# Optimization experiments

Hardware: AMD Instinct MI355X
Metric: run time of the kernel (lower is better)

## Reference

```python
import jax, jax.numpy as jnp
import numpy as np


def setup_inputs() -> dict:
    key = jax.random.key(0)
    B, C, H, W = 8, 64, 64, 64
    x = jax.random.normal(key, (B, C, H, W), dtype=jnp.float32)
    return {"x": x}


def reference(x) -> jnp.ndarray:
    # x: (B, C, H, W). Spatial self-attention over N = H*W positions with
    # Q = K = V = flattened x, no scaling, no projections (the Conv2d in the
    # original __init__ is never used in forward).
    B, C, H, W = x.shape
    N = H * W
    f = x.reshape(B, C, N)  # (B, C, N)
    # att[b, n, m] = sum_c f[b, c, n] * f[b, c, m]  -> (B, N, N)
    att = jnp.einsum('bcn,bcm->bnm', f, f)
    att = jax.nn.softmax(att, axis=-1)
    # outp[b, c, n] = sum_m f[b, c, m] * att[b, n, m]^T  (f_x @ att)
    outp = jnp.einsum('bcm,bmn->bcn', f, att).reshape(B, C, H, W)
    return x + outp
```

## Files before the change

### kernel.cpp

```cpp
#include <hip/hip_runtime.h>

typedef short v8s __attribute__((ext_vector_type(8)));
typedef short v4s __attribute__((ext_vector_type(4)));
typedef float v4f __attribute__((ext_vector_type(4)));

#define LOG2E 1.44269504088896340736f

#define WS_FBF_T 0u
#define WS_FBF   4194304u
#define WS_G     8388608u
#define WS_MAXN  8519680u
#define WS_NEED  8519712u

__device__ __forceinline__ unsigned short f2bf_rne(float f) {
  unsigned int u = __builtin_bit_cast(unsigned int, f);
  u += 0x7FFFu + ((u >> 16) & 1u);
  return (unsigned short)(u >> 16);
}

__global__ __launch_bounds__(256) void prep_kernel(
    const float* __restrict__ x, unsigned short* __restrict__ fbf_t,
    unsigned short* __restrict__ fbf, float* __restrict__ g, int* __restrict__ maxn) {
  __shared__ unsigned short T[64 * 72];
  __shared__ float red[16][64];
  const int t = threadIdx.x;
  const int b = blockIdx.x & 7;
  const int n0 = (blockIdx.x >> 3) << 6;
  const int nn = (t & 15) << 2;
  float ps0 = 0.f, ps1 = 0.f, ps2 = 0.f, ps3 = 0.f;
#pragma unroll
  for (int j = 0; j < 4; ++j) {
    int c = (t >> 4) + j * 16;
    size_t gidx = ((size_t)(b * 64 + c) << 12) + (unsigned)(n0 + nn);
    float4 v = *(const float4*)(x + gidx);
    ushort4 w;
    w.x = f2bf_rne(v.x); w.y = f2bf_rne(v.y); w.z = f2bf_rne(v.z); w.w = f2bf_rne(v.w);
    *(ushort4*)(fbf + gidx) = w;
    T[(nn + 0) * 72 + c] = w.x;
    T[(nn + 1) * 72 + c] = w.y;
    T[(nn + 2) * 72 + c] = w.z;
    T[(nn + 3) * 72 + c] = w.w;
    ps0 += v.x * v.x; ps1 += v.y * v.y; ps2 += v.z * v.z; ps3 += v.w * v.w;
  }
  red[t >> 4][nn + 0] = ps0; red[t >> 4][nn + 1] = ps1;
  red[t >> 4][nn + 2] = ps2; red[t >> 4][nn + 3] = ps3;
  __syncthreads();
  if (t < 64) {
    float gs = 0.f;
#pragma unroll
    for (int i = 0; i < 16; ++i) gs += red[i][t];
    g[b * 4096 + n0 + t] = gs;
    float m = gs;
    m = fmaxf(m, __shfl_xor(m, 1, 64));
    m = fmaxf(m, __shfl_xor(m, 2, 64));
    m = fmaxf(m, __shfl_xor(m, 4, 64));
    m = fmaxf(m, __shfl_xor(m, 8, 64));
    m = fmaxf(m, __shfl_xor(m, 16, 64));
    m = fmaxf(m, __shfl_xor(m, 32, 64));
    if (t == 0) atomicMax(maxn + b, __float_as_int(m));
  }
#pragma unroll
  for (int i = 0; i < 2; ++i) {
    int idx = t + i * 256;
    int n = idx >> 3, cs = (idx & 7) << 3;
    *(v8s*)(fbf_t + (((size_t)b << 12) + (unsigned)(n0 + n)) * 64 + cs) =
        *(const v8s*)&T[n * 72 + cs];
  }
}

__global__ __launch_bounds__(512, 2) void chanattn_main(
    const float* __restrict__ x, const unsigned short* __restrict__ fbf_t,
    const unsigned short* __restrict__ fbf, const float* __restrict__ g,
    const int* __restrict__ maxn, float* __restrict__ out) {
  __shared__ __align__(16) unsigned char smem[37888];
  unsigned short* sKt = (unsigned short*)smem;
  unsigned short* sVc = (unsigned short*)(smem + 18432);
  float* lred = (float*)(smem + 35840);

  const int tid = threadIdx.x;
  const int wave = tid >> 6, lane = tid & 63, quad = lane >> 4, l15 = lane & 15;
  const int qg = wave >> 2, kg = wave & 3;
  const int b = blockIdx.x & 7, qt = blockIdx.x >> 3;

  const unsigned short* fT = fbf_t + ((size_t)b << 18);
  const unsigned short* fV = fbf + ((size_t)b << 18);

  const int sKey = tid >> 3, sC = (tid & 7) << 3;
  const int vC = tid >> 4, vK = (tid & 15) << 3;
  const int vSlot = (vK & ~31) + ((vK & 8) ? 16 : 0) + ((vK & 16) ? 4 : 0);

#pragma unroll
  for (int i = 0; i < 2; ++i)
    *(v8s*)&sKt[(sKey + i * 64) * 72 + sC] =
        *(const v8s*)&fT[(size_t)(qt * 128 + sKey + i * 64) * 64 + sC];

  v8s pfk[2], pfv[2];
#pragma unroll
  for (int i = 0; i < 2; ++i)
    pfk[i] = *(const v8s*)&fT[(size_t)(sKey + i * 64) * 64 + sC];
#pragma unroll
  for (int i = 0; i < 2; ++i)
    pfv[i] = *(const v8s*)&fV[(size_t)(vC + i * 32) * 4096 + vK];

  __syncthreads();
  v8s bQ[4][2];
#pragma unroll
  for (int jq = 0; jq < 4; ++jq)
#pragma unroll
    for (int cs = 0; cs < 2; ++cs)
      bQ[jq][cs] = *(const v8s*)&sKt[(qg * 64 + jq * 16 + l15) * 72 + cs * 32 + quad * 8];

  float msc[4];
  {
    const float gmax = __int_as_float(maxn[b]);
#pragma unroll
    for (int jq = 0; jq < 4; ++jq) {
      int row = qt * 128 + qg * 64 + jq * 16 + l15;
      msc[jq] = __builtin_sqrtf(g[b * 4096 + row] * gmax) * LOG2E;
    }
  }
  __syncthreads();

#pragma unroll
  for (int i = 0; i < 2; ++i)
    *(v8s*)&sKt[(sKey + i * 64) * 72 + sC] = pfk[i];
#pragma unroll
  for (int i = 0; i < 2; ++i) {
    v4s lo, hi;
#pragma unroll
    for (int j = 0; j < 4; ++j) { lo[j] = pfv[i][j]; hi[j] = pfv[i][j + 4]; }
    *(v4s*)&sVc[(vC + i * 32) * 136 + vSlot] = lo;
    *(v4s*)&sVc[(vC + i * 32) * 136 + vSlot + 8] = hi;
  }

  v4f oacc[4][4];
  float rsum[4];
#pragma unroll
  for (int ct = 0; ct < 4; ++ct)
#pragma unroll
    for (int jq = 0; jq < 4; ++jq) oacc[ct][jq] = (v4f){0.f, 0.f, 0.f, 0.f};
#pragma unroll
  for (int jq = 0; jq < 4; ++jq) rsum[jq] = 0.f;

  for (int kt = 0; kt < 32; ++kt) {
    __syncthreads();

    if (kt + 1 < 32) {
      const int k0 = (kt + 1) * 128;
#pragma unroll
      for (int i = 0; i < 2; ++i)
        pfk[i] = *(const v8s*)&fT[(size_t)(k0 + sKey + i * 64) * 64 + sC];
#pragma unroll
      for (int i = 0; i < 2; ++i)
        pfv[i] = *(const v8s*)&fV[(size_t)(vC + i * 32) * 4096 + k0 + vK];
    }

    v8s aK[2][2];
#pragma unroll
    for (int t = 0; t < 2; ++t)
#pragma unroll
      for (int cs = 0; cs < 2; ++cs)
        aK[t][cs] =
            *(const v8s*)&sKt[(kg * 32 + t * 16 + l15) * 72 + cs * 32 + quad * 8];
    v8s aV[4];
#pragma unroll
    for (int ct = 0; ct < 4; ++ct)
      aV[ct] = *(const v8s*)&sVc[(ct * 16 + l15) * 136 + kg * 32 + quad * 8];

    __syncthreads();

    if (kt + 1 < 32) {
#pragma unroll
      for (int i = 0; i < 2; ++i)
        *(v8s*)&sKt[(sKey + i * 64) * 72 + sC] = pfk[i];
#pragma unroll
      for (int i = 0; i < 2; ++i) {
        v4s lo, hi;
#pragma unroll
        for (int j = 0; j < 4; ++j) { lo[j] = pfv[i][j]; hi[j] = pfv[i][j + 4]; }
        *(v4s*)&sVc[(vC + i * 32) * 136 + vSlot] = lo;
        *(v4s*)&sVc[(vC + i * 32) * 136 + vSlot + 8] = hi;
      }
    }

#pragma unroll
    for (int jq = 0; jq < 4; ++jq) {
      v4f s0 = (v4f){0.f, 0.f, 0.f, 0.f};
      v4f s1 = (v4f){0.f, 0.f, 0.f, 0.f};
#pragma unroll
      for (int cs = 0; cs < 2; ++cs) {
        s0 = __builtin_amdgcn_mfma_f32_16x16x32_bf16(aK[0][cs], bQ[jq][cs], s0, 0, 0, 0);
        s1 = __builtin_amdgcn_mfma_f32_16x16x32_bf16(aK[1][cs], bQ[jq][cs], s1, 0, 0, 0);
      }
      float p0[4], p1[4];
#pragma unroll
      for (int r = 0; r < 4; ++r) {
        p0[r] = __builtin_amdgcn_exp2f(__builtin_fmaf(s0[r], LOG2E, -msc[jq]));
        p1[r] = __builtin_amdgcn_exp2f(__builtin_fmaf(s1[r], LOG2E, -msc[jq]));
      }
      rsum[jq] += ((p0[0] + p0[1]) + (p0[2] + p0[3])) +
                  ((p1[0] + p1[1]) + (p1[2] + p1[3]));
      uint4 up;
      up.x = (__builtin_bit_cast(unsigned int, p0[1]) & 0xFFFF0000u) |
             (__builtin_bit_cast(unsigned int, p0[0]) >> 16);
      up.y = (__builtin_bit_cast(unsigned int, p0[3]) & 0xFFFF0000u) |
             (__builtin_bit_cast(unsigned int, p0[2]) >> 16);
      up.z = (__builtin_bit_cast(unsigned int, p1[1]) & 0xFFFF0000u) |
             (__builtin_bit_cast(unsigned int, p1[0]) >> 16);
      up.w = (__builtin_bit_cast(unsigned int, p1[3]) & 0xFFFF0000u) |
             (__builtin_bit_cast(unsigned int, p1[2]) >> 16);
      v8s bp = __builtin_bit_cast(v8s, up);
#pragma unroll
      for (int ct = 0; ct < 4; ++ct)
        oacc[ct][jq] =
            __builtin_amdgcn_mfma_f32_16x16x32_bf16(aV[ct], bp, oacc[ct][jq], 0, 0, 0);
    }
  }

#pragma unroll
  for (int jq = 0; jq < 4; ++jq) {
    float s = rsum[jq];
    s += __shfl_xor(s, 16, 64);
    s += __shfl_xor(s, 32, 64);
    rsum[jq] = s;
  }
  if (quad == 0) {
#pragma unroll
    for (int jq = 0; jq < 4; ++jq)
      lred[(qg * 64 + jq * 16 + l15) * 4 + kg] = rsum[jq];
  }
  __syncthreads();
  float inv[4];
#pragma unroll
  for (int jq = 0; jq < 4; ++jq) {
    const float4 lv = *(const float4*)&lred[(qg * 64 + jq * 16 + l15) * 4];
    inv[jq] = __builtin_amdgcn_rcpf((lv.x + lv.y) + (lv.z + lv.w));
  }

  float* Obuf = (float*)smem;
#pragma unroll
  for (int round = 0; round < 4; ++round) {
    if (kg == round) {
#pragma unroll
      for (int ct = 0; ct < 4; ++ct)
#pragma unroll
        for (int jq = 0; jq < 4; ++jq)
#pragma unroll
          for (int r = 0; r < 4; ++r) {
            float val = oacc[ct][jq][r] * inv[jq];
            float* p = &Obuf[(qg * 64 + ct * 16 + quad * 4 + r) * 68 + jq * 16 + l15];
            if (round == 0) *p = val; else *p += val;
          }
    }
    __syncthreads();
  }
#pragma unroll
  for (int j = 0; j < 4; ++j) {
    int idx = tid + j * 512;
    int qg2 = idx >> 10, c = (idx >> 4) & 63, q4 = idx & 15;
    const float4 o = *(const float4*)&Obuf[(qg2 * 64 + c) * 68 + q4 * 4];
    size_t gidx = ((size_t)(b * 64 + c) << 12) + (unsigned)(qt * 128 + qg2 * 64 + q4 * 4);
    const float4 xv = *(const float4*)(x + gidx);
    float4 rv;
    rv.x = xv.x + o.x; rv.y = xv.y + o.y; rv.z = xv.z + o.z; rv.w = xv.w + o.w;
    *(float4*)(out + gidx) = rv;
  }
}

__global__ __launch_bounds__(512) void
chanattn_fallback(const float* __restrict__ x, float* __restrict__ out) {
  __shared__ __align__(16) unsigned char smem[54272];
  unsigned short* sKt = (unsigned short*)smem;
  unsigned short* sVc = (unsigned short*)(smem + 18432);
  unsigned short* sP  = (unsigned short*)(smem + 35840);
  const int tid = threadIdx.x;
  const int wave = tid >> 6, lane = tid & 63, quad = lane >> 4, l15 = lane & 15;
  const int b = blockIdx.x & 7, qt = blockIdx.x >> 3;
  const float* fb = x + (size_t)b * (64 * 4096);
  const int skey = tid & 127, sc0 = (tid >> 7) << 4;
  {
    float vq[16];
#pragma unroll
    for (int j = 0; j < 16; ++j) vq[j] = fb[(sc0 + j) * 4096 + qt * 128 + skey];
    unsigned short us[16];
#pragma unroll
    for (int j = 0; j < 16; ++j) us[j] = f2bf_rne(vq[j]);
#pragma unroll
    for (int h = 0; h < 2; ++h) {
      v8s t;
#pragma unroll
      for (int j = 0; j < 8; ++j) t[j] = (short)us[h * 8 + j];
      *(v8s*)&sKt[skey * 72 + sc0 + h * 8] = t;
    }
  }
  float vk[16];
#pragma unroll
  for (int j = 0; j < 16; ++j) vk[j] = fb[(sc0 + j) * 4096 + skey];
  __syncthreads();
  v8s aq[2];
#pragma unroll
  for (int cs = 0; cs < 2; ++cs)
    aq[cs] = *(const v8s*)&sKt[(wave * 16 + l15) * 72 + cs * 32 + quad * 8];
  __syncthreads();
  v4f oacc[4];
#pragma unroll
  for (int ct = 0; ct < 4; ++ct) oacc[ct] = (v4f){0.f, 0.f, 0.f, 0.f};
  float m_run[4], l_run[4];
#pragma unroll
  for (int r = 0; r < 4; ++r) { m_run[r] = -3.0e38f; l_run[r] = 0.f; }
  unsigned short* sPw = sP + wave * (16 * 72);
  for (int kt = 0; kt < 32; ++kt) {
    {
      unsigned short us[16];
#pragma unroll
      for (int j = 0; j < 16; ++j) us[j] = f2bf_rne(vk[j]);
#pragma unroll
      for (int h = 0; h < 2; ++h) {
        v8s t;
#pragma unroll
        for (int j = 0; j < 8; ++j) t[j] = (short)us[h * 8 + j];
        *(v8s*)&sKt[skey * 72 + sc0 + h * 8] = t;
      }
#pragma unroll
      for (int j = 0; j < 16; ++j) sVc[(sc0 + j) * 136 + skey] = us[j];
    }
    __syncthreads();
    if (kt + 1 < 32) {
      const int m0 = (kt + 1) * 128;
#pragma unroll
      for (int j = 0; j < 16; ++j) vk[j] = fb[(sc0 + j) * 4096 + m0 + skey];
    }
    v4f sacc[8];
#pragma unroll
    for (int t = 0; t < 8; ++t) {
      v4f acc = (v4f){0.f, 0.f, 0.f, 0.f};
#pragma unroll
      for (int cs = 0; cs < 2; ++cs) {
        v8s bf = *(const v8s*)&sKt[(t * 16 + l15) * 72 + cs * 32 + quad * 8];
        acc = __builtin_amdgcn_mfma_f32_16x16x32_bf16(aq[cs], bf, acc, 0, 0, 0);
      }
      sacc[t] = acc;
    }
    float alpha[4], msc[4], rsum[4];
#pragma unroll
    for (int r = 0; r < 4; ++r) {
      float mv = sacc[0][r];
#pragma unroll
      for (int t = 1; t < 8; ++t) mv = fmaxf(mv, sacc[t][r]);
      mv = fmaxf(mv, __shfl_xor(mv, 8, 64));
      mv = fmaxf(mv, __shfl_xor(mv, 4, 64));
      mv = fmaxf(mv, __shfl_xor(mv, 2, 64));
      mv = fmaxf(mv, __shfl_xor(mv, 1, 64));
      float mnew = fmaxf(m_run[r], mv);
      alpha[r] = __builtin_amdgcn_exp2f((m_run[r] - mnew) * LOG2E);
      m_run[r] = mnew;
      msc[r] = mnew * LOG2E;
      l_run[r] *= alpha[r];
      rsum[r] = 0.f;
    }
#pragma unroll
    for (int ct = 0; ct < 4; ++ct)
#pragma unroll
      for (int r = 0; r < 4; ++r) oacc[ct][r] *= alpha[r];
#pragma unroll
    for (int half = 0; half < 2; ++half) {
#pragma unroll
      for (int t = half * 4; t < half * 4 + 4; ++t)
#pragma unroll
        for (int r = 0; r < 4; ++r) {
          float p = __builtin_amdgcn_exp2f(__builtin_fmaf(sacc[t][r], LOG2E, -msc[r]));
          rsum[r] += p;
          sPw[(quad * 4 + r) * 72 + (t - half * 4) * 16 + l15] = f2bf_rne(p);
        }
      asm volatile("s_waitcnt lgkmcnt(0)" ::: "memory");
#pragma unroll
      for (int ms = 0; ms < 2; ++ms) {
        v8s af = *(const v8s*)&sPw[l15 * 72 + ms * 32 + quad * 8];
#pragma unroll
        for (int ct = 0; ct < 4; ++ct) {
          v8s bf = *(const v8s*)&sVc[(ct * 16 + l15) * 136 + (half * 2 + ms) * 32 + quad * 8];
          oacc[ct] = __builtin_amdgcn_mfma_f32_16x16x32_bf16(af, bf, oacc[ct], 0, 0, 0);
        }
      }
      asm volatile("s_waitcnt lgkmcnt(0)" ::: "memory");
    }
#pragma unroll
    for (int r = 0; r < 4; ++r) {
      float s = rsum[r];
      s += __shfl_xor(s, 8, 64);
      s += __shfl_xor(s, 4, 64);
      s += __shfl_xor(s, 2, 64);
      s += __shfl_xor(s, 1, 64);
      l_run[r] += s;
    }
    __syncthreads();
  }
  float inv[4];
#pragma unroll
  for (int r = 0; r < 4; ++r) inv[r] = __builtin_amdgcn_rcpf(l_run[r]);
  float* sOt = (float*)smem;
#pragma unroll
  for (int ct = 0; ct < 4; ++ct)
#pragma unroll
    for (int r = 0; r < 4; ++r)
      sOt[(ct * 16 + l15) * 132 + wave * 16 + quad * 4 + r] = oacc[ct][r] * inv[r];
  __syncthreads();
#pragma unroll
  for (int j = 0; j < 4; ++j) {
    int idx = tid + j * 512;
    int nv = idx & 31, c = idx >> 5;
    float4 o = *(const float4*)&sOt[c * 132 + nv * 4];
    size_t gaddr = (size_t)b * (64 * 4096) + (size_t)c * 4096 + (size_t)(qt * 128 + nv * 4);
    float4 xv = *(const float4*)(x + gaddr);
    float4 res = make_float4(xv.x + o.x, xv.y + o.y, xv.z + o.z, xv.w + o.w);
    *(float4*)(out + gaddr) = res;
  }
}

extern "C" void kernel_launch(void* const* d_in, const int* in_sizes, int n_in,
                              void* d_out, int out_size, void* d_ws, size_t ws_size,
                              hipStream_t stream) {
  const float* xin = (const float*)d_in[0];
  float* out = (float*)d_out;
  if (ws_size >= (size_t)WS_NEED) {
    unsigned short* fbf_t = (unsigned short*)((char*)d_ws + WS_FBF_T);
    unsigned short* fbf = (unsigned short*)((char*)d_ws + WS_FBF);
    float* g = (float*)((char*)d_ws + WS_G);
    int* maxn = (int*)((char*)d_ws + WS_MAXN);
    hipMemsetAsync(maxn, 0, 8 * sizeof(int), stream);
    prep_kernel<<<dim3(512), dim3(256), 0, stream>>>(xin, fbf_t, fbf, g, maxn);
    chanattn_main<<<dim3(256), dim3(512), 0, stream>>>(xin, fbf_t, fbf, g, maxn, out);
  } else {
    chanattn_fallback<<<dim3(256), dim3(512), 0, stream>>>(xin, out);
  }
}
```

Before: 118.2 us.

## Double-buffer K/V tiles in LDS and replace atomic max with per-block partials

The main loop now keeps two LDS buffers for the key and value tiles. Each iteration runs one barrier instead of two, and global prefetch runs two tiles ahead, with the store for the next tile placed after the first query sub-tile's MFMAs. The per-batch max norm is no longer built with a memset plus atomicMax. Prep blocks write partial maxima that the main kernel reduces with wave shuffles. This removes a memset launch and the atomics, but nearly doubles LDS use per block (to 72KB), which may limit occupancy at two 512-thread blocks per CU.

```diff
diff --git a/kernel.cpp b/kernel.cpp
--- a/kernel.cpp
+++ b/kernel.cpp
@@ -9,8 +9,8 @@
 #define WS_FBF_T 0u
 #define WS_FBF   4194304u
 #define WS_G     8388608u
-#define WS_MAXN  8519680u
-#define WS_NEED  8519712u
+#define WS_BMAX  8519680u
+#define WS_NEED  8521728u
 
 __device__ __forceinline__ unsigned short f2bf_rne(float f) {
   unsigned int u = __builtin_bit_cast(unsigned int, f);
@@ -20,7 +20,7 @@
 
 __global__ __launch_bounds__(256) void prep_kernel(
     const float* __restrict__ x, unsigned short* __restrict__ fbf_t,
-    unsigned short* __restrict__ fbf, float* __restrict__ g, int* __restrict__ maxn) {
+    unsigned short* __restrict__ fbf, float* __restrict__ g, float* __restrict__ bmax) {
   __shared__ unsigned short T[64 * 72];
   __shared__ float red[16][64];
   const int t = threadIdx.x;
@@ -57,7 +57,7 @@
     m = fmaxf(m, __shfl_xor(m, 8, 64));
     m = fmaxf(m, __shfl_xor(m, 16, 64));
     m = fmaxf(m, __shfl_xor(m, 32, 64));
-    if (t == 0) atomicMax(maxn + b, __float_as_int(m));
+    if (t == 0) bmax[b * 64 + (blockIdx.x >> 3)] = m;
   }
 #pragma unroll
   for (int i = 0; i < 2; ++i) {
@@ -71,11 +71,12 @@
 __global__ __launch_bounds__(512, 2) void chanattn_main(
     const float* __restrict__ x, const unsigned short* __restrict__ fbf_t,
     const unsigned short* __restrict__ fbf, const float* __restrict__ g,
-    const int* __restrict__ maxn, float* __restrict__ out) {
-  __shared__ __align__(16) unsigned char smem[37888];
-  unsigned short* sKt = (unsigned short*)smem;
-  unsigned short* sVc = (unsigned short*)(smem + 18432);
-  float* lred = (float*)(smem + 35840);
+    const float* __restrict__ bmax, float* __restrict__ out) {
+  __shared__ __align__(16) unsigned char smem[73728];
+  unsigned short* sKtB = (unsigned short*)smem;
+  unsigned short* sVcB = (unsigned short*)(smem + 18432);
+  float* lred = (float*)(smem + 71680);
+  const int BUF = 17920;
 
   const int tid = threadIdx.x;
   const int wave = tid >> 6, lane = tid & 63, quad = lane >> 4, l15 = lane & 15;
@@ -89,11 +90,22 @@
   const int vC = tid >> 4, vK = (tid & 15) << 3;
   const int vSlot = (vK & ~31) + ((vK & 8) ? 16 : 0) + ((vK & 16) ? 4 : 0);
 
-#pragma unroll
-  for (int i = 0; i < 2; ++i)
-    *(v8s*)&sKt[(sKey + i * 64) * 72 + sC] =
+  float gm = bmax[b * 64 + lane];
+  gm = fmaxf(gm, __shfl_xor(gm, 1, 64));
+  gm = fmaxf(gm, __shfl_xor(gm, 2, 64));
+  gm = fmaxf(gm, __shfl_xor(gm, 4, 64));
+  gm = fmaxf(gm, __shfl_xor(gm, 8, 64));
+  gm = fmaxf(gm, __shfl_xor(gm, 16, 64));
+  gm = fmaxf(gm, __shfl_xor(gm, 32, 64));
+  float gq[4];
+#pragma unroll
+  for (int jq = 0; jq < 4; ++jq)
+    gq[jq] = g[b * 4096 + qt * 128 + qg * 64 + jq * 16 + l15];
+
+#pragma unroll
+  for (int i = 0; i < 2; ++i)
+    *(v8s*)&sKtB[(sKey + i * 64) * 72 + sC] =
         *(const v8s*)&fT[(size_t)(qt * 128 + sKey + i * 64) * 64 + sC];
-
   v8s pfk[2], pfv[2];
 #pragma unroll
   for (int i = 0; i < 2; ++i)
@@ -108,30 +120,29 @@
   for (int jq = 0; jq < 4; ++jq)
 #pragma unroll
     for (int cs = 0; cs < 2; ++cs)
-      bQ[jq][cs] = *(const v8s*)&sKt[(qg * 64 + jq * 16 + l15) * 72 + cs * 32 + quad * 8];
-
+      bQ[jq][cs] = *(const v8s*)&sKtB[(qg * 64 + jq * 16 + l15) * 72 + cs * 32 + quad * 8];
   float msc[4];
-  {
-    const float gmax = __int_as_float(maxn[b]);
-#pragma unroll
-    for (int jq = 0; jq < 4; ++jq) {
-      int row = qt * 128 + qg * 64 + jq * 16 + l15;
-      msc[jq] = __builtin_sqrtf(g[b * 4096 + row] * gmax) * LOG2E;
-    }
-  }
-  __syncthreads();
-
-#pragma unroll
-  for (int i = 0; i < 2; ++i)
-    *(v8s*)&sKt[(sKey + i * 64) * 72 + sC] = pfk[i];
+#pragma unroll
+  for (int jq = 0; jq < 4; ++jq) msc[jq] = __builtin_sqrtf(gq[jq] * gm) * LOG2E;
+  __syncthreads();
+
+#pragma unroll
+  for (int i = 0; i < 2; ++i)
+    *(v8s*)&sKtB[(sKey + i * 64) * 72 + sC] = pfk[i];
 #pragma unroll
   for (int i = 0; i < 2; ++i) {
     v4s lo, hi;
 #pragma unroll
     for (int j = 0; j < 4; ++j) { lo[j] = pfv[i][j]; hi[j] = pfv[i][j + 4]; }
-    *(v4s*)&sVc[(vC + i * 32) * 136 + vSlot] = lo;
-    *(v4s*)&sVc[(vC + i * 32) * 136 + vSlot + 8] = hi;
-  }
+    *(v4s*)&sVcB[(vC + i * 32) * 136 + vSlot] = lo;
+    *(v4s*)&sVcB[(vC + i * 32) * 136 + vSlot + 8] = hi;
+  }
+#pragma unroll
+  for (int i = 0; i < 2; ++i)
+    pfk[i] = *(const v8s*)&fT[(size_t)(128 + sKey + i * 64) * 64 + sC];
+#pragma unroll
+  for (int i = 0; i < 2; ++i)
+    pfv[i] = *(const v8s*)&fV[(size_t)(vC + i * 32) * 4096 + 128 + vK];
 
   v4f oacc[4][4];
   float rsum[4];
@@ -144,9 +155,68 @@
 
   for (int kt = 0; kt < 32; ++kt) {
     __syncthreads();
-
-    if (kt + 1 < 32) {
-      const int k0 = (kt + 1) * 128;
+    const int po = (kt & 1) * BUF;
+    const int pn = ((kt & 1) ^ 1) * BUF;
+
+    v8s aK[2][2];
+#pragma unroll
+    for (int t = 0; t < 2; ++t)
+#pragma unroll
+      for (int cs = 0; cs < 2; ++cs)
+        aK[t][cs] =
+            *(const v8s*)&sKtB[po + (kg * 32 + t * 16 + l15) * 72 + cs * 32 + quad * 8];
+    v8s aV[4];
+#pragma unroll
+    for (int ct = 0; ct < 4; ++ct)
+      aV[ct] = *(const v8s*)&sVcB[po + (ct * 16 + l15) * 136 + kg * 32 + quad * 8];
+
+    {
+      const int jq = 0;
+      v4f s0 = (v4f){0.f, 0.f, 0.f, 0.f}, s1 = (v4f){0.f, 0.f, 0.f, 0.f};
+#pragma unroll
+      for (int cs = 0; cs < 2; ++cs) {
+        s0 = __builtin_amdgcn_mfma_f32_16x16x32_bf16(aK[0][cs], bQ[jq][cs], s0, 0, 0, 0);
+        s1 = __builtin_amdgcn_mfma_f32_16x16x32_bf16(aK[1][cs], bQ[jq][cs], s1, 0, 0, 0);
+      }
+      float p0[4], p1[4];
+#pragma unroll
+      for (int r = 0; r < 4; ++r) {
+        p0[r] = __builtin_amdgcn_exp2f(__builtin_fmaf(s0[r], LOG2E, -msc[jq]));
+        p1[r] = __builtin_amdgcn_exp2f(__builtin_fmaf(s1[r], LOG2E, -msc[jq]));
+      }
+      rsum[jq] += ((p0[0] + p0[1]) + (p0[2] + p0[3])) +
+                  ((p1[0] + p1[1]) + (p1[2] + p1[3]));
+      uint4 up;
+      up.x = (__builtin_bit_cast(unsigned int, p0[1]) & 0xFFFF0000u) |
+             (__builtin_bit_cast(unsigned int, p0[0]) >> 16);
+      up.y = (__builtin_bit_cast(unsigned int, p0[3]) & 0xFFFF0000u) |
+             (__builtin_bit_cast(unsigned int, p0[2]) >> 16);
+      up.z = (__builtin_bit_cast(unsigned int, p1[1]) & 0xFFFF0000u) |
+             (__builtin_bit_cast(unsigned int, p1[0]) >> 16);
+      up.w = (__builtin_bit_cast(unsigned int, p1[3]) & 0xFFFF0000u) |
+             (__builtin_bit_cast(unsigned int, p1[2]) >> 16);
+      v8s bp = __builtin_bit_cast(v8s, up);
+#pragma unroll
+      for (int ct = 0; ct < 4; ++ct)
+        oacc[ct][jq] =
+            __builtin_amdgcn_mfma_f32_16x16x32_bf16(aV[ct], bp, oacc[ct][jq], 0, 0, 0);
+    }
+
+    if (kt < 31) {
+#pragma unroll
+      for (int i = 0; i < 2; ++i)
+        *(v8s*)&sKtB[pn + (sKey + i * 64) * 72 + sC] = pfk[i];
+#pragma unroll
+      for (int i = 0; i < 2; ++i) {
+        v4s lo, hi;
+#pragma unroll
+        for (int j = 0; j < 4; ++j) { lo[j] = pfv[i][j]; hi[j] = pfv[i][j + 4]; }
+        *(v4s*)&sVcB[pn + (vC + i * 32) * 136 + vSlot] = lo;
+        *(v4s*)&sVcB[pn + (vC + i * 32) * 136 + vSlot + 8] = hi;
+      }
+    }
+    if (kt < 30) {
+      const int k0 = (kt + 2) << 7;
 #pragma unroll
       for (int i = 0; i < 2; ++i)
         pfk[i] = *(const v8s*)&fT[(size_t)(k0 + sKey + i * 64) * 64 + sC];
@@ -155,38 +225,9 @@
         pfv[i] = *(const v8s*)&fV[(size_t)(vC + i * 32) * 4096 + k0 + vK];
     }
 
-    v8s aK[2][2];
-#pragma unroll
-    for (int t = 0; t < 2; ++t)
-#pragma unroll
-      for (int cs = 0; cs < 2; ++cs)
-        aK[t][cs] =
-            *(const v8s*)&sKt[(kg * 32 + t * 16 + l15) * 72 + cs * 32 + quad * 8];
-    v8s aV[4];
-#pragma unroll
-    for (int ct = 0; ct < 4; ++ct)
-      aV[ct] = *(const v8s*)&sVc[(ct * 16 + l15) * 136 + kg * 32 + quad * 8];
-
-    __syncthreads();
-
-    if (kt + 1 < 32) {
-#pragma unroll
-      for (int i = 0; i < 2; ++i)
-        *(v8s*)&sKt[(sKey + i * 64) * 72 + sC] = pfk[i];
-#pragma unroll
-      for (int i = 0; i < 2; ++i) {
-        v4s lo, hi;
-#pragma unroll
-        for (int j = 0; j < 4; ++j) { lo[j] = pfv[i][j]; hi[j] = pfv[i][j + 4]; }
-        *(v4s*)&sVc[(vC + i * 32) * 136 + vSlot] = lo;
-        *(v4s*)&sVc[(vC + i * 32) * 136 + vSlot + 8] = hi;
-      }
-    }
-
-#pragma unroll
-    for (int jq = 0; jq < 4; ++jq) {
-      v4f s0 = (v4f){0.f, 0.f, 0.f, 0.f};
-      v4f s1 = (v4f){0.f, 0.f, 0.f, 0.f};
+#pragma unroll
+    for (int jq = 1; jq < 4; ++jq) {
+      v4f s0 = (v4f){0.f, 0.f, 0.f, 0.f}, s1 = (v4f){0.f, 0.f, 0.f, 0.f};
 #pragma unroll
       for (int cs = 0; cs < 2; ++cs) {
         s0 = __builtin_amdgcn_mfma_f32_16x16x32_bf16(aK[0][cs], bQ[jq][cs], s0, 0, 0, 0);
@@ -426,10 +467,9 @@
     unsigned short* fbf_t = (unsigned short*)((char*)d_ws + WS_FBF_T);
     unsigned short* fbf = (unsigned short*)((char*)d_ws + WS_FBF);
     float* g = (float*)((char*)d_ws + WS_G);
-    int* maxn = (int*)((char*)d_ws + WS_MAXN);
-    hipMemsetAsync(maxn, 0, 8 * sizeof(int), stream);
-    prep_kernel<<<dim3(512), dim3(256), 0, stream>>>(xin, fbf_t, fbf, g, maxn);
-    chanattn_main<<<dim3(256), dim3(512), 0, stream>>>(xin, fbf_t, fbf, g, maxn, out);
+    float* bmax = (float*)((char*)d_ws + WS_BMAX);
+    prep_kernel<<<dim3(512), dim3(256), 0, stream>>>(xin, fbf_t, fbf, g, bmax);
+    chanattn_main<<<dim3(256), dim3(512), 0, stream>>>(xin, fbf_t, fbf, g, bmax, out);
   } else {
     chanattn_fallback<<<dim3(256), dim3(512), 0, stream>>>(xin, out);
   }
```

New measurement: 105.0 us. 1.13x faster.
